# Optimization experiments

Measured on AMD Instinct MI355X. Metric: run time of the kernel, lower is better.

The kernel has to match this reference:

```python
import jax, jax.numpy as jnp
import numpy as np

NUM_TASKS, IN_SIZE, OUT_SIZE, N_ROWS = 64, 512, 512, 2048


def setup_inputs() -> dict:
    key = jax.random.key(0)
    k_x, k_t, k_w = jax.random.split(key, 3)
    inputs = jax.random.normal(k_x, (N_ROWS, IN_SIZE), dtype=jnp.float32)
    task_ids = jax.random.randint(k_t, (N_ROWS,), 0, NUM_TASKS, dtype=jnp.int64)
    # in_size == out_size path: identity + N(0, 0.03) perturbation per task
    W = (jnp.eye(IN_SIZE, OUT_SIZE, dtype=jnp.float32)[None]
         + 0.03 * jax.random.normal(k_w, (NUM_TASKS, IN_SIZE, OUT_SIZE), dtype=jnp.float32))
    return {"inputs": inputs, "task_ids": task_ids, "W": W}


def reference(inputs, task_ids, W):
    # Gather the full per-row weight matrix then batched vector-matrix multiply,
    # faithful to torch.einsum('ni,nio->no', inputs, W[task_ids]).
    aligned = W[task_ids]                       # [I, in, out]
    return jnp.einsum("ni,nio->no", inputs, aligned)  # [I, out]
```

## Files before the change

### kernel.cpp

```cpp
#include <hip/hip_runtime.h>


#define NDIM 512
#define KDIM 512
#define NCOL 32
#define KH   256
#define GRID 512
#define NUNIT 2

typedef _Float16 f16x8 __attribute__((ext_vector_type(8)));
typedef float    f32x4 __attribute__((ext_vector_type(4)));
typedef int      i32x4 __attribute__((ext_vector_type(4)));

__global__ __launch_bounds__(256, 2) void k_fused4(
    const float* __restrict__ x,
    const int*   __restrict__ tids,
    const float* __restrict__ W,
    float*       __restrict__ out,
    int n_rows)
{
    const int tid  = threadIdx.x;
    const int lane = tid & 63;
    const int wv   = tid >> 6;
    const int ml   = lane & 15;
    const int q    = lane >> 4;
    const int sc4  = (tid & 7) * 4;
    const int ob   = tid >> 3;

    __shared__ __align__(16) _Float16 Wt[2][NCOL * KH];
    __shared__ unsigned short rlw[4 * 128];

    const int rbase = wv * 512 + lane * 8;
    int tval[8];
    if (rbase + 7 < n_rows) {
        const i32x4 a = *(const i32x4*)(tids + rbase);
        const i32x4 b = *(const i32x4*)(tids + rbase + 4);
        tval[0] = a[0]; tval[1] = a[1]; tval[2] = a[2]; tval[3] = a[3];
        tval[4] = b[0]; tval[5] = b[1]; tval[6] = b[2]; tval[7] = b[3];
    } else {
        #pragma unroll
        for (int j = 0; j < 8; ++j)
            tval[j] = (rbase + j < n_rows) ? tids[rbase + j] : -1;
    }

    int   cloc = 0;
    int   c0   = 0;
    const float* xr = x;
    float4 wr[8];

    auto issueW = [&](const float* Wg, int h) {
        #pragma unroll
        for (int j = 0; j < 8; ++j)
            wr[j] = *(const float4*)(Wg + (size_t)(h * KH + ob * 8 + j) * NDIM + sc4);
    };

    auto stageW = [&](int t) {
        #pragma unroll
        for (int j2 = 0; j2 < 4; ++j2) {
            f16x8 h8;
            #pragma unroll
            for (int j = 0; j < 8; ++j)
                h8[j] = (_Float16)(((const float*)&wr[j])[j2]);
            const int c  = sc4 + j2;
            const int po = ob ^ (c & 7);
            *(f16x8*)&Wt[t][c * KH + po * 8] = h8;
        }
    };

    auto load_half = [&](const float* xrp, int t, f16x8* paf) {
        #pragma unroll
        for (int h = 0; h < 2; ++h) {
            f32x4 xa[8];
            #pragma unroll
            for (int k2 = 0; k2 < 4; ++k2) {
                const int ks = h * 4 + k2;
                xa[2 * k2]     = *(const f32x4*)(xrp + t * KH + ks * 32 + q * 8);
                xa[2 * k2 + 1] = *(const f32x4*)(xrp + t * KH + ks * 32 + q * 8 + 4);
            }
            #pragma unroll
            for (int k2 = 0; k2 < 4; ++k2) {
                f16x8 af;
                const float* a0 = (const float*)&xa[2 * k2];
                #pragma unroll
                for (int j = 0; j < 8; ++j) af[j] = (_Float16)a0[j];
                paf[h * 4 + k2] = af;
            }
        }
    };

    auto mma_half = [&](int t, const f16x8* paf, f32x4* acc) {
        #pragma unroll
        for (int ks = 0; ks < 8; ++ks) {
            #pragma unroll
            for (int ct = 0; ct < 2; ++ct) {
                const int cB = ct * 16 + ml;
                const int po = (ks * 4 + q) ^ (cB & 7);
                const f16x8 bf = *(const f16x8*)&Wt[t][cB * KH + po * 8];
                acc[ct] = __builtin_amdgcn_mfma_f32_16x16x32_f16(paf[ks], bf, acc[ct], 0, 0, 0);
            }
        }
    };

    auto store_rows = [&](int g0, const f32x4* acc) {
        #pragma unroll
        for (int rg = 0; rg < 4; ++rg) {
            const int pos = g0 + q * 4 + rg;
            if (pos < cloc) {
                float* op = out + (size_t)rlw[wv * 128 + pos] * NDIM + c0 + ml;
                op[0]  = acc[0][rg];
                op[16] = acc[1][rg];
            }
        }
    };

    int task = (blockIdx.x & 7) | ((blockIdx.x >> 7) << 3);
    c0 = ((blockIdx.x >> 3) & 15) * NCOL;
    const float* Wg = W + (size_t)task * KDIM * NDIM + c0;
    issueW(Wg, 0);

    #pragma unroll
    for (int uu = 0; uu < NUNIT; ++uu) {
        cloc = 0;
        #pragma unroll
        for (int j = 0; j < 8; ++j) {
            const bool m = (tval[j] == task);
            const unsigned long long bal = __ballot(m);
            const int rank = __popcll(bal & ((1ull << lane) - 1ull));
            if (m) rlw[wv * 128 + cloc + rank] = (unsigned short)(rbase + j);
            cloc += __popcll(bal);
        }

        f16x8 pafA[8], pafB[8];
        if (cloc > 0) {
            const int idx = (ml < cloc) ? ml : (cloc - 1);
            xr = x + (size_t)rlw[wv * 128 + idx] * KDIM;
            load_half(xr, 0, pafA);
        }

        stageW(0);
        issueW(Wg, 1);
        asm volatile("s_waitcnt lgkmcnt(0)" ::: "memory");
        __builtin_amdgcn_s_barrier();
        __builtin_amdgcn_sched_barrier(0);

        f32x4 acc[2] = {};
        if (cloc > 0) mma_half(0, pafA, acc);
        if (cloc > 0) load_half(xr, 1, pafB);
        stageW(1);

        int ntask = 0, nc0 = 0;
        const float* nWg = nullptr;
        if (uu + 1 < NUNIT) {
            const int nu = blockIdx.x + (uu + 1) * GRID;
            ntask = (nu & 7) | ((nu >> 7) << 3);
            nc0   = ((nu >> 3) & 15) * NCOL;
            nWg   = W + (size_t)ntask * KDIM * NDIM + nc0;
            issueW(nWg, 0);
        }

        asm volatile("s_waitcnt lgkmcnt(0)" ::: "memory");
        __builtin_amdgcn_s_barrier();
        __builtin_amdgcn_sched_barrier(0);

        if (cloc > 0) {
            mma_half(1, pafB, acc);
            store_rows(0, acc);
        }

        for (int g0 = 16; g0 < cloc; g0 += 16) {
            const int idx = g0 + ml;
            const float* xr2 = x + (size_t)rlw[wv * 128 + ((idx < cloc) ? idx : (cloc - 1))] * KDIM;
            f16x8 pf[8];
            f32x4 a2[2] = {};
            load_half(xr2, 0, pf);
            mma_half(0, pf, a2);
            load_half(xr2, 1, pf);
            mma_half(1, pf, a2);
            store_rows(g0, a2);
        }

        if (uu + 1 < NUNIT) {
            asm volatile("s_waitcnt lgkmcnt(0)" ::: "memory");
            __builtin_amdgcn_s_barrier();
            __builtin_amdgcn_sched_barrier(0);
            task = ntask; c0 = nc0; Wg = nWg;
        }
    }
}

extern "C" void kernel_launch(void* const* d_in, const int* in_sizes, int n_in,
                              void* d_out, int out_size, void* d_ws, size_t ws_size,
                              hipStream_t stream) {
    const float* x    = (const float*)d_in[0];
    const int*   tids = (const int*)d_in[1];
    const float* W    = (const float*)d_in[2];
    float*       out  = (float*)d_out;
    const int n_rows  = in_sizes[1];

    k_fused4<<<dim3(GRID), dim3(256), 0, stream>>>(x, tids, W, out, n_rows);
}
```

Before: 105.3 us.

## Double-buffer W register prefetch across both K halves and work units

```diff
diff --git a/kernel.cpp b/kernel.cpp
--- a/kernel.cpp
+++ b/kernel.cpp
@@ -6,13 +6,12 @@
 #define NCOL 32
 #define KH   256
 #define GRID 512
-#define NUNIT 2
 
 typedef _Float16 f16x8 __attribute__((ext_vector_type(8)));
 typedef float    f32x4 __attribute__((ext_vector_type(4)));
 typedef int      i32x4 __attribute__((ext_vector_type(4)));
 
-__global__ __launch_bounds__(256, 2) void k_fused4(
+__global__ __launch_bounds__(256, 2) void k_fused5(
     const float* __restrict__ x,
     const int*   __restrict__ tids,
     const float* __restrict__ W,
@@ -46,24 +45,37 @@
     int   cloc = 0;
     int   c0   = 0;
     const float* xr = x;
-    float4 wr[8];
-
-    auto issueW = [&](const float* Wg, int h) {
+
+    float4 wrE[8], wrO[8];
+
+    auto issueW = [&](const float* Wg, int h, float4 (&wrb)[8]) {
         #pragma unroll
         for (int j = 0; j < 8; ++j)
-            wr[j] = *(const float4*)(Wg + (size_t)(h * KH + ob * 8 + j) * NDIM + sc4);
-    };
-
-    auto stageW = [&](int t) {
+            wrb[j] = *(const float4*)(Wg + (size_t)(h * KH + ob * 8 + j) * NDIM + sc4);
+    };
+
+    auto stageW = [&](int t, const float4 (&wrb)[8]) {
         #pragma unroll
         for (int j2 = 0; j2 < 4; ++j2) {
             f16x8 h8;
             #pragma unroll
             for (int j = 0; j < 8; ++j)
-                h8[j] = (_Float16)(((const float*)&wr[j])[j2]);
+                h8[j] = (_Float16)(((const float*)&wrb[j])[j2]);
             const int c  = sc4 + j2;
             const int po = ob ^ (c & 7);
             *(f16x8*)&Wt[t][c * KH + po * 8] = h8;
+        }
+    };
+
+    auto do_scan = [&](int task) {
+        cloc = 0;
+        #pragma unroll
+        for (int j = 0; j < 8; ++j) {
+            const bool m = (tval[j] == task);
+            const unsigned long long bal = __ballot(m);
+            const int rank = __popcll(bal & ((1ull << lane) - 1ull));
+            if (m) rlw[wv * 128 + cloc + rank] = (unsigned short)(rbase + j);
+            cloc += __popcll(bal);
         }
     };
 
@@ -113,60 +125,7 @@
         }
     };
 
-    int task = (blockIdx.x & 7) | ((blockIdx.x >> 7) << 3);
-    c0 = ((blockIdx.x >> 3) & 15) * NCOL;
-    const float* Wg = W + (size_t)task * KDIM * NDIM + c0;
-    issueW(Wg, 0);
-
-    #pragma unroll
-    for (int uu = 0; uu < NUNIT; ++uu) {
-        cloc = 0;
-        #pragma unroll
-        for (int j = 0; j < 8; ++j) {
-            const bool m = (tval[j] == task);
-            const unsigned long long bal = __ballot(m);
-            const int rank = __popcll(bal & ((1ull << lane) - 1ull));
-            if (m) rlw[wv * 128 + cloc + rank] = (unsigned short)(rbase + j);
-            cloc += __popcll(bal);
-        }
-
-        f16x8 pafA[8], pafB[8];
-        if (cloc > 0) {
-            const int idx = (ml < cloc) ? ml : (cloc - 1);
-            xr = x + (size_t)rlw[wv * 128 + idx] * KDIM;
-            load_half(xr, 0, pafA);
-        }
-
-        stageW(0);
-        issueW(Wg, 1);
-        asm volatile("s_waitcnt lgkmcnt(0)" ::: "memory");
-        __builtin_amdgcn_s_barrier();
-        __builtin_amdgcn_sched_barrier(0);
-
-        f32x4 acc[2] = {};
-        if (cloc > 0) mma_half(0, pafA, acc);
-        if (cloc > 0) load_half(xr, 1, pafB);
-        stageW(1);
-
-        int ntask = 0, nc0 = 0;
-        const float* nWg = nullptr;
-        if (uu + 1 < NUNIT) {
-            const int nu = blockIdx.x + (uu + 1) * GRID;
-            ntask = (nu & 7) | ((nu >> 7) << 3);
-            nc0   = ((nu >> 3) & 15) * NCOL;
-            nWg   = W + (size_t)ntask * KDIM * NDIM + nc0;
-            issueW(nWg, 0);
-        }
-
-        asm volatile("s_waitcnt lgkmcnt(0)" ::: "memory");
-        __builtin_amdgcn_s_barrier();
-        __builtin_amdgcn_sched_barrier(0);
-
-        if (cloc > 0) {
-            mma_half(1, pafB, acc);
-            store_rows(0, acc);
-        }
-
+    auto extras = [&]() {
         for (int g0 = 16; g0 < cloc; g0 += 16) {
             const int idx = g0 + ml;
             const float* xr2 = x + (size_t)rlw[wv * 128 + ((idx < cloc) ? idx : (cloc - 1))] * KDIM;
@@ -178,14 +137,83 @@
             mma_half(1, pf, a2);
             store_rows(g0, a2);
         }
-
-        if (uu + 1 < NUNIT) {
-            asm volatile("s_waitcnt lgkmcnt(0)" ::: "memory");
-            __builtin_amdgcn_s_barrier();
-            __builtin_amdgcn_sched_barrier(0);
-            task = ntask; c0 = nc0; Wg = nWg;
-        }
-    }
+    };
+
+    const int id0 = blockIdx.x, id1 = blockIdx.x + GRID;
+    const int task0 = (id0 & 7) | ((id0 >> 7) << 3);
+    const int c00   = ((id0 >> 3) & 15) * NCOL;
+    const int task1 = (id1 & 7) | ((id1 >> 7) << 3);
+    const int c01   = ((id1 >> 3) & 15) * NCOL;
+    const float* Wg0 = W + (size_t)task0 * KDIM * NDIM + c00;
+    const float* Wg1 = W + (size_t)task1 * KDIM * NDIM + c01;
+
+    issueW(Wg0, 0, wrE);
+    issueW(Wg0, 1, wrO);
+
+    f16x8 pafA[8], pafB[8];
+    f32x4 acc[2];
+
+    do_scan(task0);
+    c0 = c00;
+    if (cloc > 0) {
+        const int idx = (ml < cloc) ? ml : (cloc - 1);
+        xr = x + (size_t)rlw[wv * 128 + idx] * KDIM;
+        load_half(xr, 0, pafA);
+    }
+
+    stageW(0, wrE);
+    issueW(Wg1, 0, wrE);
+    asm volatile("s_waitcnt lgkmcnt(0)" ::: "memory");
+    __builtin_amdgcn_s_barrier();
+    __builtin_amdgcn_sched_barrier(0);
+
+    acc[0] = (f32x4){}; acc[1] = (f32x4){};
+    if (cloc > 0) mma_half(0, pafA, acc);
+    if (cloc > 0) load_half(xr, 1, pafB);
+
+    stageW(1, wrO);
+    issueW(Wg1, 1, wrO);
+    asm volatile("s_waitcnt lgkmcnt(0)" ::: "memory");
+    __builtin_amdgcn_s_barrier();
+    __builtin_amdgcn_sched_barrier(0);
+
+    if (cloc > 0) {
+        mma_half(1, pafB, acc);
+        store_rows(0, acc);
+    }
+    extras();
+
+    asm volatile("s_waitcnt lgkmcnt(0)" ::: "memory");
+    __builtin_amdgcn_s_barrier();
+    __builtin_amdgcn_sched_barrier(0);
+
+    do_scan(task1);
+    c0 = c01;
+    if (cloc > 0) {
+        const int idx = (ml < cloc) ? ml : (cloc - 1);
+        xr = x + (size_t)rlw[wv * 128 + idx] * KDIM;
+        load_half(xr, 0, pafA);
+    }
+
+    stageW(0, wrE);
+    asm volatile("s_waitcnt lgkmcnt(0)" ::: "memory");
+    __builtin_amdgcn_s_barrier();
+    __builtin_amdgcn_sched_barrier(0);
+
+    acc[0] = (f32x4){}; acc[1] = (f32x4){};
+    if (cloc > 0) mma_half(0, pafA, acc);
+    if (cloc > 0) load_half(xr, 1, pafB);
+
+    stageW(1, wrO);
+    asm volatile("s_waitcnt lgkmcnt(0)" ::: "memory");
+    __builtin_amdgcn_s_barrier();
+    __builtin_amdgcn_sched_barrier(0);
+
+    if (cloc > 0) {
+        mma_half(1, pafB, acc);
+        store_rows(0, acc);
+    }
+    extras();
 }
 
 extern "C" void kernel_launch(void* const* d_in, const int* in_sizes, int n_in,
@@ -197,5 +225,5 @@
     float*       out  = (float*)d_out;
     const int n_rows  = in_sizes[1];
 
-    k_fused4<<<dim3(GRID), dim3(256), 0, stream>>>(x, tids, W, out, n_rows);
+    k_fused5<<<dim3(GRID), dim3(256), 0, stream>>>(x, tids, W, out, n_rows);
 }
```

Result: no change. 105.9 us (+0.6%).
